# Optimization experiments

Hardware: AMD Instinct MI355X
Metric: run time of the kernel (lower is better)

Reference implementation:

```python
import jax, jax.numpy as jnp
import numpy as np

# block index -> upsample target resolution / whether self-attention is applied
RES = [32, 64, 256, 128, 64, 32, 16, 16, 32, 64, 128, 256]
ATTN = [False, False, False, False, False, True, True, True, True, False, False, False]
EPS = 1e-5


def conv5(x, w, b):
    # valid 5x5 conv, NCHW
    y = jax.lax.conv_general_dilated(x, w, (1, 1), 'VALID',
                                     dimension_numbers=('NCHW', 'OIHW', 'NCHW'))
    return y + b[None, :, None, None]


def up_nearest(x, size):
    # torch nn.Upsample(size) nearest: src_idx = floor(dst_idx * in / out)
    H, W = x.shape[2], x.shape[3]
    ri = (jnp.arange(size) * H) // size
    ci = (jnp.arange(size) * W) // size
    return x[:, :, ri][:, :, :, ci]


def norm_hw(x):
    # InstanceNorm2d(affine=False) == LayerNorm((H,W)) with identity affine:
    # normalize over spatial dims per (N, C), biased variance.
    m = x.mean((2, 3), keepdims=True)
    v = x.var((2, 3), keepdims=True)
    return (x - m) * jax.lax.rsqrt(v + EPS)


def norm_batch(x):
    # BatchNorm2d in training mode: batch statistics over (N, H, W) per channel.
    m = x.mean((0, 2, 3), keepdims=True)
    v = x.var((0, 2, 3), keepdims=True)
    return (x - m) * jax.lax.rsqrt(v + EPS)


def attention(x, qw, qb, kw, kb, vw, vb):
    B, C, H, W = x.shape
    q = (jnp.einsum('oc,bchw->bohw', qw, x) + qb[None, :, None, None]).reshape(B, C, H * W)
    k = (jnp.einsum('oc,bchw->bohw', kw, x) + kb[None, :, None, None]).reshape(B, C, H * W)
    v = (jnp.einsum('oc,bchw->bohw', vw, x) + vb[None, :, None, None]).reshape(B, C, H * W)
    # scores[b, m, n] = sum_c k[b, c, m] * q[b, c, n]; softmax over n
    a = jax.nn.softmax(jnp.einsum('bcm,bcn->bmn', k, q), axis=-1)  # [B, HW, HW]
    out = jnp.einsum('bcm,bmn->bcn', v, a).reshape(B, C, H, W)
    return out + x


def setup_inputs() -> dict:
    key = jax.random.key(0)
    k = jax.random.split(key, 22)
    s = 0.1
    f = jnp.float32
    return {
        'x': jax.random.normal(k[0], (32, 3, 256, 256), f),
        'noise_z': jax.random.normal(k[1], (1, 512), f),
        'lin_w': jax.random.normal(k[2], (768, 512), f) * 0.02,
        'lin_b': jax.random.normal(k[3], (768,), f) * 0.02,
        'conv_w': jax.random.normal(k[4], (12, 3, 3, 5, 5), f) * s,
        'conv_b': jax.random.normal(k[5], (12, 3), f) * s,
        'conv2_w': jax.random.normal(k[6], (12, 3, 3, 5, 5), f) * s,
        'conv2_b': jax.random.normal(k[7], (12, 3), f) * s,
        'q_w': jax.random.normal(k[8], (12, 3, 3), f) * s,
        'q_b': jax.random.normal(k[9], (12, 3), f) * s,
        'k_w': jax.random.normal(k[10], (12, 3, 3), f) * s,
        'k_b': jax.random.normal(k[11], (12, 3), f) * s,
        'v_w': jax.random.normal(k[12], (12, 3, 3), f) * s,
        'v_b': jax.random.normal(k[13], (12, 3), f) * s,
        'in_p': jax.random.uniform(k[14], (12, 3), f),
        'ln_p': jax.random.uniform(k[15], (12, 3), f),
        'bn_p': jax.random.uniform(k[16], (12, 3), f),
        'bn_w': jax.random.uniform(k[17], (12, 3), f),
        'bn_b': jax.random.uniform(k[18], (12, 3), f) * 0.1,
        'p1': jax.random.uniform(k[19], (12,), f),
        'p2': jax.random.uniform(k[20], (12,), f),
    }


def reference(x, noise_z, lin_w, lin_b, conv_w, conv_b, conv2_w, conv2_b,
              q_w, q_b, k_w, k_b, v_w, v_b, in_p, ln_p, bn_p, bn_w, bn_b, p1, p2):

    def block(i, h):
        r = RES[i]
        real = h
        y = up_nearest(conv5(real, conv_w[i], conv_b[i]), r)
        # InstanceNorm / LayerNorm (no affine) coincide here; BatchNorm has affine.
        inorm = norm_hw(y)
        bnorm = norm_batch(y) * bn_w[i][None, :, None, None] + bn_b[i][None, :, None, None]
        y2 = y + (jnp.sum(in_p[i]) + jnp.sum(ln_p[i])) * inorm + jnp.sum(bn_p[i]) * bnorm
        y2 = y2 * p1[i] + p2[i] * up_nearest(conv5(real, conv2_w[i], conv2_b[i]), r)
        if ATTN[i]:
            y2 = attention(y2, q_w[i], q_b[i], k_w[i], k_b[i], v_w[i], v_b[i])
        return y2

    # noise path: Linear(512 -> 768) -> (1, 3, 16, 16) -> ReesBlock(32) -> ReesBlock(64)
    n = (noise_z @ lin_w.T + lin_b).reshape(1, 3, 16, 16)
    n = block(0, n)
    n = block(1, n)  # (1, 3, 64, 64)

    a = x
    for i in range(2, 12):
        a = block(i, a)
        if i == 4:  # encoder index 2, resolution 64 -> add noise (broadcast over batch)
            a = a + n
    return jnp.tanh(a)
```

## Files before the change

kernel.cpp:

```cpp
#include <hip/hip_runtime.h>
#include <math.h>

#define EPS 1e-5f
#define LOG2E 1.44269504088896340736f

#define AS_GLOBAL __attribute__((address_space(1)))
#define AS_LDS    __attribute__((address_space(3)))

__device__ __forceinline__ float2 ab_from(float s1, float s2, float bs, float bs2,
    float hw, float Nf, float si_, float sb, float bnw_c, float bnb_c, float p1v) {
  float inv = 1.0f / hw;
  float mi = s1 * inv, vi = s2 * inv - mi * mi;
  float ri = rsqrtf(vi + EPS);
  float invb = 1.0f / (Nf * hw);
  float mb = bs * invb, vb = bs2 * invb - mb * mb;
  float rb = rsqrtf(vb + EPS);
  float A = 1.0f + si_ * ri + sb * rb * bnw_c;
  float B = -(si_ * ri * mi + sb * rb * bnw_c * mb) + sb * bnb_c;
  return make_float2(A * p1v, B * p1v);
}

__device__ __forceinline__ void compute_AB_P(
    const float* __restrict__ P, int n, int NT, int T, float hw, float Nf,
    const float* __restrict__ inp, const float* __restrict__ lnp,
    const float* __restrict__ bnp, const float* __restrict__ bnw,
    const float* __restrict__ bnb, const float* __restrict__ p1p,
    const float* __restrict__ p2p, float* pA, float* pB, float* pP2,
    float* sred ) {
  int t = threadIdx.x;
  if (t == 0) *pP2 = p2p[0];
  if (t < 192) {
    int c2 = t >> 5, l = t & 31;
    const float* pp = P + c2 * NT;
    float aAll = 0.f, aOwn = 0.f;
    int base = n * T;
    #pragma unroll 4
    for (int i = l; i < NT; i += 32) {
      float v = pp[i];
      aAll += v;
      if ((unsigned)(i - base) < (unsigned)T) aOwn += v;
    }
    #pragma unroll
    for (int off = 16; off; off >>= 1) {
      aAll += __shfl_down(aAll, off, 32);
      aOwn += __shfl_down(aOwn, off, 32);
    }
    if (l == 0) { sred[c2] = aOwn; sred[6 + c2] = aAll; }
  }
  __syncthreads();
  if (t < 3) {
    int c = t;
    float si_ = inp[0] + inp[1] + inp[2] + lnp[0] + lnp[1] + lnp[2];
    float sb = bnp[0] + bnp[1] + bnp[2];
    float2 ab = ab_from(sred[2 * c], sred[2 * c + 1], sred[6 + 2 * c],
                        sred[6 + 2 * c + 1], hw, Nf, si_, sb, bnw[c], bnb[c],
                        p1p[0]);
    pA[c] = ab.x;
    pB[c] = ab.y;
  }
  __syncthreads();
}

#define STATS_REDUCE_STORE(scv, sqv, sumsp, bidv)                             \
  {                                                                           \
    _Pragma("unroll")                                                         \
    for (int off = 32; off; off >>= 1) {                                      \
      _Pragma("unroll")                                                       \
      for (int c = 0; c < 3; ++c) {                                           \
        scv[c] += __shfl_down(scv[c], off);                                   \
        sqv[c] += __shfl_down(sqv[c], off);                                   \
      }                                                                       \
    }                                                                         \
    __shared__ float redS[4][3], redQ[4][3];                                  \
    int wid = threadIdx.x >> 6, lane = threadIdx.x & 63;                      \
    if (lane == 0) {                                                          \
      _Pragma("unroll")                                                       \
      for (int c = 0; c < 3; ++c) { redS[wid][c] = scv[c]; redQ[wid][c] = sqv[c]; } \
    }                                                                         \
    __syncthreads();                                                          \
    if (threadIdx.x < 3) {                                                    \
      int c = threadIdx.x;                                                    \
      int NTg = (int)gridDim.x;                                               \
      sumsp[(2 * c) * NTg + (bidv)] =                                         \
          redS[0][c] + redS[1][c] + redS[2][c] + redS[3][c];                  \
      sumsp[(2 * c + 1) * NTg + (bidv)] =                                     \
          redQ[0][c] + redQ[1][c] + redQ[2][c] + redQ[3][c];                  \
    }                                                                         \
  }

__device__ __forceinline__ int xcd_swz() {
// ... 54 lines not shown
    int gx2 = sx0 + col2; gx2 = gx2 < Hin ? gx2 : Hin - 1;
    int gy = sy0 + rr; gy = gy < Hin ? gy : Hin - 1;
    lin[(cc * IHv + rr) * IW + col2] =
        stage_val<MODE, IDENT>(inb, ps, pyu, pbase, Hin, gy, gx2, Sp, logrp,
                               pA, pB, pP2v, pnoise, cc);
  }
}

template <int SMODE, int THv>
__global__ __launch_bounds__(256) void conv_up_t(
    const float* __restrict__ in, const float2* __restrict__ pyu,
    float2* __restrict__ yu,
    const float* __restrict__ w1, const float* __restrict__ b1,
    const float* __restrict__ w2, const float* __restrict__ b2,
    float* __restrict__ sums, int Hin, int S, int r, int tilesX, int tilesY,
    const float* __restrict__ psums,
    const float* __restrict__ pinp, const float* __restrict__ plnp,
    const float* __restrict__ pbnp, const float* __restrict__ pbnw,
    const float* __restrict__ pbnb, const float* __restrict__ pp1,
    const float* __restrict__ pp2, const float* __restrict__ pnoise,
    int pN, int Sp, int logrp, int pNT, int pT) {
  const int TW = 64, IW = 68, IH = THv + 4, NH = THv / 16;
  __shared__ float lin[3 * IH * IW];
  __shared__ float pA[3], pB[3], pP2v, sred[12];
  int bid = xcd_swz();
  int tpi = tilesX * tilesY;
  int n = bid / tpi;
  int trem = bid - n * tpi;
  int tyB = trem / tilesX, txB = trem - tyB * tilesX;
  int px0 = txB * TW, py0 = tyB * THv;
  const float* inb = in + (size_t)n * 3 * Hin * Hin;
  if (SMODE == 1) {
    compute_AB_P(psums, n, pNT, pT, (float)(Hin * Hin), (float)pN, pinp, plnp,
                 pbnp, pbnw, pbnb, pp1, pp2, pA, pB, &pP2v, sred);
    size_t pbase = (size_t)n * 3 * Sp * Sp;
    stage_tile<1, false, IH>(lin, nullptr, 0, pyu, pbase, Hin, py0, px0, Sp,
                             logrp, pA, pB, pP2v, pnoise);
  } else if (SMODE == 3) {
    const float* smallb = in + (size_t)n * 3 * Sp * Sp;
    stage_tile<3, false, IH>(lin, smallb, 0, nullptr, 0, Hin, py0, px0, Sp,
                             logrp, nullptr, nullptr, 0.f, nullptr);
  } else {
    if (px0 + IW <= Hin && py0 + IH <= Hin) {
      for (int t4 = threadIdx.x; t4 < 3 * IH * 17; t4 += 256) {
        int cc = t4 / (IH * 17);
        int rem = t4 - cc * (IH * 17);
        int rr = rem / 17, j = rem - rr * 17;
        const float* src = inb + ((size_t)cc * Hin + py0 + rr) * Hin + px0 + 4 * j;
        int base = t4 - (threadIdx.x & 63);
// ... 71 lines not shown
        float2* yp = yu + idx;
        *reinterpret_cast<float4*>(yp) =
            make_float4(a1[h][c][0], a2[h][c][0], a1[h][c][1], a2[h][c][1]);
        *reinterpret_cast<float4*>(yp + 2) =
            make_float4(a1[h][c][2], a2[h][c][2], a1[h][c][3], a2[h][c][3]);
        #pragma unroll
        for (int x = 0; x < 4; ++x) {
          float wgt = wy * wx[x];
          sc[c] += a1[h][c][x] * wgt;
          sq[c] += a1[h][c][x] * a1[h][c][x] * wgt;
        }
      }
    }
  }
  STATS_REDUCE_STORE(sc, sq, sums, bid)
}

template <int SMODE, bool IDENT, int THv>
__global__ __launch_bounds__(256) void conv_dn_t(
    const float* __restrict__ in, const float2* __restrict__ pyu,
    float2* __restrict__ yu,
    const float* __restrict__ w1, const float* __restrict__ b1,
    const float* __restrict__ w2, const float* __restrict__ b2,
    float* __restrict__ sums, int Hin, int S, int hc, int logr,
    int tilesX, int tilesY,
    const float* __restrict__ psums,
    const float* __restrict__ pinp, const float* __restrict__ plnp,
    const float* __restrict__ pbnp, const float* __restrict__ pbnw,
    const float* __restrict__ pbnb, const float* __restrict__ pp1,
    const float* __restrict__ pp2, const float* __restrict__ pnoise,
    int pN, int Sp, int logrp, int pNT, int pT) {
  const int TW = 32, IW = 68, IH = (THv == 16) ? 36 : 20, NH = THv / 8;
  __shared__ float lin[3 * IH * IW];
  __shared__ float pA[3], pB[3], pP2v, sred[12];
  int bid = xcd_swz();
  int tpi = tilesX * tilesY;
  int n = bid / tpi;
  int trem = bid - n * tpi;
  int tyB = trem / tilesX, txB = trem - tyB * tilesX;
  int px0 = txB * TW, py0 = tyB * THv;
  int sy0 = (py0 * hc) >> logr, sx0 = (px0 * hc) >> logr;
  const float* inb = in + (size_t)n * 3 * Hin * Hin;
  if (SMODE == 1) {
    compute_AB_P(psums, n, pNT, pT, (float)(Hin * Hin), (float)pN, pinp, plnp,
                 pbnp, pbnw, pbnb, pp1, pp2, pA, pB, &pP2v, sred);
    size_t pbase = (size_t)n * 3 * Sp * Sp;
    stage_tile<1, IDENT, IH>(lin, nullptr, 0, pyu, pbase, Hin, sy0, sx0, Sp,
                             logrp, pA, pB, pP2v, pnoise);
  } else if (SMODE == 2) {
    size_t ps = (size_t)96 * Hin * Hin;
    stage_tile<2, false, IH>(lin, inb, ps, nullptr, 0, Hin, sy0, sx0, 0, 0,
                             nullptr, nullptr, 0.f, nullptr);
  } else {
    stage_tile<0, false, IH>(lin, inb, 0, nullptr, 0, Hin, sy0, sx0, 0, 0,
                             nullptr, nullptr, 0.f, nullptr);
  }
  __syncthreads();
  int tx = threadIdx.x & 31, ty = threadIdx.x >> 5;
  int px = px0 + tx;
  int sxl = ((px * hc) >> logr) - sx0;
  int pys[NH], syl[NH];
  #pragma unroll
  for (int h = 0; h < NH; ++h) {
    pys[h] = py0 + ty + 8 * h;
    syl[h] = ((pys[h] * hc) >> logr) - sy0;
  }
  float a1[NH][3], a2[NH][3];
  #pragma unroll
  for (int h = 0; h < NH; ++h)
    #pragma unroll
    for (int c = 0; c < 3; ++c) { a1[h][c] = b1[c]; a2[h][c] = b2[c]; }
  #pragma unroll
  for (int ci = 0; ci < 3; ++ci) {
    const float* wp1 = w1 + ci * 25;
    const float* wp2 = w2 + ci * 25;
    #pragma unroll
    for (int h = 0; h < NH; ++h) {
      const float* lrow = lin + (ci * IH + syl[h]) * IW + sxl;
      #pragma unroll
      for (int ky = 0; ky < 5; ++ky) {
        float v[5];
        #pragma unroll
        for (int j = 0; j < 5; ++j) v[j] = lrow[ky * IW + j];
        #pragma unroll
        for (int c = 0; c < 3; ++c) {
          #pragma unroll
          for (int kx = 0; kx < 5; ++kx) {
            a1[h][c] = fmaf(v[kx], wp1[c * 75 + ky * 5 + kx], a1[h][c]);
            a2[h][c] = fmaf(v[kx], wp2[c * 75 + ky * 5 + kx], a2[h][c]);
          }
        }
      }
    }
  }
  float sc[3] = {0.f, 0.f, 0.f}, sq[3] = {0.f, 0.f, 0.f};
  #pragma unroll
  for (int h = 0; h < NH; ++h) {
    bool valid = (pys[h] < S) && (px < S);
    if (valid) {
      #pragma unroll
      for (int c = 0; c < 3; ++c) {
        size_t idx = ((size_t)(n * 3 + c) * S + pys[h]) * S + px;
        yu[idx] = make_float2(a1[h][c], a2[h][c]);
        sc[c] += a1[h][c];
        sq[c] += a1[h][c] * a1[h][c];
      }
    }
  }
  STATS_REDUCE_STORE(sc, sq, sums, bid)
}

__global__ __launch_bounds__(256) void linear_wave(
    const float* __restrict__ z, const float* __restrict__ w,
    const float* __restrict__ b, float* __restrict__ out) {
  int row = (blockIdx.x << 2) + (threadIdx.x >> 6);
  int lane = threadIdx.x & 63;
  const float4* wr = reinterpret_cast<const float4*>(w + (size_t)row * 512);
  const float4* zz = reinterpret_cast<const float4*>(z);
  float acc = 0.f;
  #pragma unroll
  for (int i = 0; i < 2; ++i) {
    float4 wv = wr[lane + 64 * i];
    float4 zv = zz[lane + 64 * i];
    acc += wv.x * zv.x + wv.y * zv.y + wv.z * zv.z + wv.w * zv.w;
// ... 139 lines not shown
    }
    __syncthreads();
  }
  {
    float P2b = p2p[1];
    for (int t = tid; t < 12288; t += 256) {
      int c = t >> 12, p = t & 4095;
      int oy = p >> 6, ox = p & 63;
      int si = ((oy * 28) >> 6) * 28 + ((ox * 28) >> 6);
      nb0[t] = AB[c] * ys1[c * 784 + si] + AB[3 + c] + P2b * u21[c * 784 + si];
    }
  }
}

__global__ __launch_bounds__(256) void attn_rows_f(
    const float2* __restrict__ yu, const float* __restrict__ sums,
    const float* __restrict__ inp, const float* __restrict__ lnp,
    const float* __restrict__ bnp, const float* __restrict__ bnw,
    const float* __restrict__ bnb, const float* __restrict__ p1p,
    const float* __restrict__ p2p,
    const float* __restrict__ qw, const float* __restrict__ qb,
    const float* __restrict__ kw, const float* __restrict__ kb,
    float* __restrict__ Mp, float* __restrict__ Lp, int S,
    int pNT, int pT) {
  __shared__ float pA[3], pB[3], pP2v, sred[12];
  __shared__ __align__(16) float y2s[768], qs[768];
  int bid = blockIdx.x;
  int np = bid & 3; bid >>= 2;
  int mc = bid & 3;
  int b = bid >> 2;
  compute_AB_P(sums, b, pNT, pT, 1024.f, 32.f, inp, lnp, bnp, bnw, bnb, p1p,
               p2p, pA, pB, &pP2v, sred);
  size_t ybase = (size_t)b * 3 * S * S;
  for (int t = threadIdx.x; t < 768; t += 256) {
    int c = t >> 8, j = t & 255;
    int n = (np << 8) + j;
    int oy = n >> 5, ox = n & 31;
    int si = ((oy * S) >> 5) * S + ((ox * S) >> 5);
    float2 v = yu[ybase + c * S * S + si];
    y2s[t] = pA[c] * v.x + pB[c] + pP2v * v.y;
  }
  __syncthreads();
  for (int t = threadIdx.x; t < 768; t += 256) {
    int o = t >> 8, j = t & 255;
    qs[t] = qb[o] + qw[o * 3] * y2s[j] + qw[o * 3 + 1] * y2s[256 + j] +
            qw[o * 3 + 2] * y2s[512 + j];
  }
// ... 27 lines not shown
  #pragma unroll 4
  for (int j = 0; j < 64; ++j) {
    float4 qa = qa4[j], qbv = qb4[j], qc = qc4[j];
    float s0 = k0 * qa.x + k1 * qbv.x + k2 * qc.x;
    float s1 = k0 * qa.y + k1 * qbv.y + k2 * qc.y;
    float s2 = k0 * qa.z + k1 * qbv.z + k2 * qc.z;
    float s3 = k0 * qa.w + k1 * qbv.w + k2 * qc.w;
    l += exp2f(s0 - mr) + exp2f(s1 - mr) + exp2f(s2 - mr) + exp2f(s3 - mr);
  }
  int idx = (b * 4 + np) * 1024 + m;
  Mp[idx] = mr;
  Lp[idx] = l;
}

__global__ __launch_bounds__(256) void attn_out_f(
    const float2* __restrict__ yu, const float* __restrict__ sums,
    const float* __restrict__ inp, const float* __restrict__ lnp,
    const float* __restrict__ bnp, const float* __restrict__ bnw,
    const float* __restrict__ bnb, const float* __restrict__ p1p,
    const float* __restrict__ p2p,
    const float* __restrict__ qw, const float* __restrict__ qb,
    const float* __restrict__ kw, const float* __restrict__ kb,
    const float* __restrict__ vw, const float* __restrict__ vb,
    const float* __restrict__ Mp, const float* __restrict__ Lp,
    float* __restrict__ aout, int S, int pNT, int pT) {
  __shared__ float pA[3], pB[3], pP2v, sred[12];
  __shared__ __align__(16) float ym[768], ks[768], vs[768], Ms[256], Ls[256];
  int bid = blockIdx.x;
  int mp = bid & 3; bid >>= 2;
  int nc = bid & 3;
  int b = bid >> 2;
  compute_AB_P(sums, b, pNT, pT, 1024.f, 32.f, inp, lnp, bnp, bnw, bnb, p1p,
               p2p, pA, pB, &pP2v, sred);
  size_t ybase = (size_t)b * 3 * S * S;
  for (int t = threadIdx.x; t < 768; t += 256) {
    int c = t >> 8, j = t & 255;
    int m = (mp << 8) + j;
    int oy = m >> 5, ox = m & 31;
    int si = ((oy * S) >> 5) * S + ((ox * S) >> 5);
    float2 v = yu[ybase + c * S * S + si];
    ym[t] = pA[c] * v.x + pB[c] + pP2v * v.y;
  }
  __syncthreads();
  for (int t = threadIdx.x; t < 768; t += 256) {
    int o = t >> 8, j = t & 255;
    float y0 = ym[j], y1 = ym[256 + j], y2v = ym[512 + j];
    ks[t] = (kb[o] + kw[o * 3] * y0 + kw[o * 3 + 1] * y1 + kw[o * 3 + 2] * y2v) * LOG2E;
    vs[t] = vb[o] + vw[o * 3] * y0 + vw[o * 3 + 1] * y1 + vw[o * 3 + 2] * y2v;
// ... 48 lines not shown
    s = ka.z * q0 + kbv.z * q1 + kc.z * q2;
    w = exp2f(s - mm.z) * ll.z;
    a0 = fmaf(va.z, w, a0); a1 = fmaf(vbv.z, w, a1); a2 = fmaf(vc.z, w, a2);
    s = ka.w * q0 + kbv.w * q1 + kc.w * q2;
    w = exp2f(s - mm.w) * ll.w;
    a0 = fmaf(va.w, w, a0); a1 = fmaf(vbv.w, w, a1); a2 = fmaf(vc.w, w, a2);
  }
  if (mp == 0) { a0 += yn[0]; a1 += yn[1]; a2 += yn[2]; }
  size_t o0 = (size_t)mp * 98304 + (size_t)b * 3072 + n;
  aout[o0] = a0;
  aout[o0 + 1024] = a1;
  aout[o0 + 2048] = a2;
}

__global__ __launch_bounds__(1024) void attn256_conv(
    const float2* __restrict__ yu, const float* __restrict__ sums,
    const float* __restrict__ inp, const float* __restrict__ lnp,
    const float* __restrict__ bnp, const float* __restrict__ bnw,
    const float* __restrict__ bnb, const float* __restrict__ p1p,
    const float* __restrict__ p2p,
    const float* __restrict__ qw, const float* __restrict__ qb,
    const float* __restrict__ kw, const float* __restrict__ kb,
    const float* __restrict__ vw, const float* __restrict__ vb,
    const float* __restrict__ cw1, const float* __restrict__ cb1,
    const float* __restrict__ cw2, const float* __restrict__ cb2,
    float2* __restrict__ yu_out, float* __restrict__ sums_out, int S, int r,
    int pNT, int pT) {
  __shared__ float pA[3], pB[3], pP2v, sred[12];
  __shared__ __align__(16) float y2s[768], qs[768], ks[768], vs[768];
  __shared__ __align__(16) float Ms[256], Ls[256];
  __shared__ float Mq[1024], Lq[1024];
  __shared__ float Oq[3072];
  __shared__ float redS[16][3], redQ[16][3];
  int tid = threadIdx.x;
  int quarter = tid >> 8;
  int lane256 = tid & 255;
  int b = blockIdx.x;
  compute_AB_P(sums, b, pNT, pT, 256.f, 32.f, inp, lnp, bnp, bnw, bnb, p1p,
               p2p, pA, pB, &pP2v, sred);
  size_t ybase = (size_t)b * 3 * S * S;
  if (tid < 768) {
    int c = tid >> 8, p = tid & 255;
    int oy = p >> 4, ox = p & 15;
    int si = ((oy * S) >> 4) * S + ((ox * S) >> 4);
    float2 v = yu[ybase + c * S * S + si];
    y2s[tid] = pA[c] * v.x + pB[c] + pP2v * v.y;
  }
  __syncthreads();
  if (tid < 768) {
    int o = tid >> 8, p = tid & 255;
    float y0 = y2s[p], y1 = y2s[256 + p], y2v = y2s[512 + p];
    qs[tid] = qb[o] + qw[o * 3] * y0 + qw[o * 3 + 1] * y1 + qw[o * 3 + 2] * y2v;
    ks[tid] = (kb[o] + kw[o * 3] * y0 + kw[o * 3 + 1] * y1 + kw[o * 3 + 2] * y2v) * LOG2E;
    vs[tid] = vb[o] + vw[o * 3] * y0 + vw[o * 3 + 1] * y1 + vw[o * 3 + 2] * y2v;
// ... 126 lines not shown
  int wid = tid >> 6, lane = tid & 63;
  if (lane == 0) {
    #pragma unroll
    for (int c = 0; c < 3; ++c) { redS[wid][c] = sc[c]; redQ[wid][c] = sq[c]; }
  }
  __syncthreads();
  if (tid < 3) {
    int c = tid;
    float s1 = 0.f, s2 = 0.f;
    #pragma unroll
    for (int w = 0; w < 16; ++w) { s1 += redS[w][c]; s2 += redQ[w][c]; }
    int NTg = (int)gridDim.x;
    sums_out[(2 * c) * NTg + b] = s1;
    sums_out[(2 * c + 1) * NTg + b] = s2;
  }
}

__global__ __launch_bounds__(256) void attn144(
    const float2* __restrict__ yu, const float* __restrict__ sums,
    const float* __restrict__ inp, const float* __restrict__ lnp,
    const float* __restrict__ bnp, const float* __restrict__ bnw,
    const float* __restrict__ bnb, const float* __restrict__ p1p,
    const float* __restrict__ p2p,
    const float* __restrict__ qw, const float* __restrict__ qb,
    const float* __restrict__ kw, const float* __restrict__ kb,
    const float* __restrict__ vw, const float* __restrict__ vb,
    float* __restrict__ O) {
  __shared__ float pA[3], pB[3], pP2v, sred[12];
  __shared__ float y2[432], qs[432], ks[432], vs[432];
  __shared__ float Ms[144], Ls[144], wn[144];
  int b = blockIdx.x;
  int tid = threadIdx.x;
  compute_AB_P(sums, b, 32, 1, 1024.f, 32.f, inp, lnp, bnp, bnw, bnb, p1p,
               p2p, pA, pB, &pP2v, sred);
  for (int t = tid; t < 432; t += 256) {
    int c = t / 144, j = t - c * 144;
    float2 v = yu[((size_t)b * 3 + c) * 144 + j];
    y2[t] = pA[c] * v.x + pB[c] + pP2v * v.y;
  }
  __syncthreads();
  if (tid < 144) {
    int j = tid;
    float y0 = y2[j], y1 = y2[144 + j], y2v = y2[288 + j];
    #pragma unroll
    for (int o = 0; o < 3; ++o) {
      qs[o * 144 + j] = qb[o] + qw[o * 3] * y0 + qw[o * 3 + 1] * y1 + qw[o * 3 + 2] * y2v;
      ks[o * 144 + j] = (kb[o] + kw[o * 3] * y0 + kw[o * 3 + 1] * y1 + kw[o * 3 + 2] * y2v) * LOG2E;
      vs[o * 144 + j] = vb[o] + vw[o * 3] * y0 + vw[o * 3 + 1] * y1 + vw[o * 3 + 2] * y2v;
    }
// ... 27 lines not shown
    for (int m = 0; m < 144; ++m) {
      float s = ks[m] * q0 + ks[144 + m] * q1 + ks[288 + m] * q2;
      float w = wn[m] * exp2f(s - Ms[m]) * Ls[m];
      a0 = fmaf(vs[m], w, a0);
      a1 = fmaf(vs[144 + m], w, a1);
      a2 = fmaf(vs[288 + m], w, a2);
    }
    size_t ob = (size_t)b * 432;
    O[ob + nq] = a0 + y2[nq];
    O[ob + 144 + nq] = a1 + y2[144 + nq];
    O[ob + 288 + nq] = a2 + y2[288 + nq];
  }
}

__global__ __launch_bounds__(256) void elem_final(
    const float2* __restrict__ yu, const float* __restrict__ sums,
    const float* __restrict__ inp, const float* __restrict__ lnp,
    const float* __restrict__ bnp, const float* __restrict__ bnw,
    const float* __restrict__ bnb, const float* __restrict__ p1p,
    const float* __restrict__ p2p, float* __restrict__ out, int S,
    int pNT, int pT) {
  __shared__ float pA[3], pB[3], pP2v, sred[12];
  int bid = xcd_swz();
  int n = bid >> 8;
  int p = ((bid & 255) << 8) + threadIdx.x;
  compute_AB_P(sums, n, pNT, pT, 65536.f, 32.f, inp, lnp, bnp, bnw, bnb, p1p,
               p2p, pA, pB, &pP2v, sred);
  int oy = p >> 8, ox = p & 255;
  int si = ((oy * S) >> 8) * S + ((ox * S) >> 8);
  size_t ybase = (size_t)n * 3 * S * S;
  #pragma unroll
  for (int c = 0; c < 3; ++c) {
    float2 v = yu[ybase + c * S * S + si];
    out[((size_t)(n * 3 + c) << 16) + p] = tanhf(pA[c] * v.x + pB[c] + pP2v * v.y);
  }
}

#define NPX nullptr, nullptr, nullptr, nullptr, nullptr, nullptr, nullptr, \
            nullptr, nullptr, 0, 0, 0, 0, 0

extern "C" void kernel_launch(void* const* d_in, const int* in_sizes, int n_in,
                              void* d_out, int out_size, void* d_ws, size_t ws_size,
                              hipStream_t stream) {
  const float* x       = (const float*)d_in[0];
  const float* noise_z = (const float*)d_in[1];
  const float* lin_w   = (const float*)d_in[2];
  const float* lin_b   = (const float*)d_in[3];
  const float* conv_w  = (const float*)d_in[4];
  const float* conv_b  = (const float*)d_in[5];
  const float* conv2_w = (const float*)d_in[6];
  const float* conv2_b = (const float*)d_in[7];
  const float* q_w     = (const float*)d_in[8];
  const float* q_b     = (const float*)d_in[9];
  const float* k_w     = (const float*)d_in[10];
  const float* k_b     = (const float*)d_in[11];
  const float* v_w     = (const float*)d_in[12];
  const float* v_b     = (const float*)d_in[13];
  const float* in_p    = (const float*)d_in[14];
  const float* ln_p    = (const float*)d_in[15];
  const float* bn_p    = (const float*)d_in[16];
  const float* bn_w    = (const float*)d_in[17];
  const float* bn_b    = (const float*)d_in[18];
  const float* p1      = (const float*)d_in[19];
  const float* p2      = (const float*)d_in[20];
  float* out = (float*)d_out;

  float* ws = (float*)d_ws;
  size_t off = 0;
  auto alloc = [&](size_t nf) { float* p = ws + off; off += nf; return p; };
  float* PS   = alloc(21120);
  float* PS2  = PS;
  float* PS3  = PS + 6144;
  float* PS4  = PS + 12288;
  float* PS5  = PS + 15360;
  float* PS6  = PS + 16128;
  float* PS6a = PS + 16512;
  float* PS7a = PS + 16704;
  float* PS9  = PS + 16896;
  float* PS10 = PS + 17280;
  float* PS11 = PS + 18048;
  float* P45  = alloc(393216);
  float* O144 = alloc(13824);
  float2* YU2 = (float2*)alloc(12192768);
  float2* PA  = (float2*)alloc(3145728);
  float2* PB  = (float2*)alloc(3145728);
  float* Mp   = alloc(131072);
  float* Lp   = alloc(131072);
  float* NB0  = alloc(12288);
  float* LIN  = alloc(768);

  const float* nul = nullptr;
  const float2* nul2 = nullptr;

  linear_wave<<<192, 256, 0, stream>>>(noise_z, lin_w, lin_b, LIN);
  noise_rest<<<1, 256, 0, stream>>>(LIN, conv_w, conv_b, conv2_w, conv2_b,
      in_p, ln_p, bn_p, bn_w, bn_b, p1, p2, NB0);

  conv_up_t<0, 32><<<1024, 256, 0, stream>>>(x, nul2, YU2, conv_w + 450,
      conv_b + 6, conv2_w + 450, conv2_b + 6, PS2, 256, 252, 256, 4, 8,
      NPX);
  conv_dn_t<1, false, 16><<<1024, 256, 0, stream>>>(nul, YU2, PA,
      conv_w + 675, conv_b + 9, conv2_w + 675, conv2_b + 9, PS3,
      256, 128, 252, 7, 4, 8,
      PS2, in_p + 6, ln_p + 6, bn_p + 6, bn_w + 6, bn_b + 6, p1 + 2,
      p2 + 2, nul, 32, 252, 8, 1024, 32);
  conv_dn_t<1, true, 8><<<512, 256, 0, stream>>>(nul, PA, PB,
      conv_w + 900, conv_b + 12, conv2_w + 900, conv2_b + 12, PS4,
      128, 64, 124, 6, 2, 8,
      PS3, in_p + 9, ln_p + 9, bn_p + 9, bn_w + 9, bn_b + 9, p1 + 3,
      p2 + 3, nul, 32, 128, 7, 1024, 32);
  conv_dn_t<1, true, 8><<<128, 256, 0, stream>>>(nul, PB, PA,
      conv_w + 1125, conv_b + 15, conv2_w + 1125, conv2_b + 15, PS5,
      64, 32, 60, 5, 1, 4,
      PS4, in_p + 12, ln_p + 12, bn_p + 12, bn_w + 12, bn_b + 12, p1 + 4,
      p2 + 4, NB0, 32, 64, 6, 512, 16);
  attn_rows_f<<<512, 256, 0, stream>>>(PA, PS5, in_p + 15, ln_p + 15,
      bn_p + 15, bn_w + 15, bn_b + 15, p1 + 5, p2 + 5,
      q_w + 45, q_b + 15, k_w + 45, k_b + 15, Mp, Lp, 32, 128, 4);
  attn_out_f<<<512, 256, 0, stream>>>(PA, PS5, in_p + 15, ln_p + 15,
      bn_p + 15, bn_w + 15, bn_b + 15, p1 + 5, p2 + 5,
      q_w + 45, q_b + 15, k_w + 45, k_b + 15, v_w + 45, v_b + 15, Mp, Lp, P45,
      32, 128, 4);
  conv_dn_t<2, false, 8><<<64, 256, 0, stream>>>(P45, nul2, PB,
      conv_w + 1350, conv_b + 18, conv2_w + 1350, conv2_b + 18, PS6,
      32, 16, 28, 4, 1, 2, NPX);
  attn256_conv<<<32, 1024, 0, stream>>>(PB, PS6, in_p + 18, ln_p + 18,
      bn_p + 18, bn_w + 18, bn_b + 18, p1 + 6, p2 + 6,
      q_w + 54, q_b + 18, k_w + 54, k_b + 18, v_w + 54, v_b + 18,
      conv_w + 1575, conv_b + 21, conv2_w + 1575, conv2_b + 21,
      PA, PS6a, 16, 16, 64, 2);
  attn256_conv<<<32, 1024, 0, stream>>>(PA, PS6a, in_p + 21, ln_p + 21,
      bn_p + 21, bn_w + 21, bn_b + 21, p1 + 7, p2 + 7,
      q_w + 63, q_b + 21, k_w + 63, k_b + 21, v_w + 63, v_b + 21,
      conv_w + 1800, conv_b + 24, conv2_w + 1800, conv2_b + 24,
      PB, PS7a, 12, 32, 32, 1);
  attn144<<<32, 256, 0, stream>>>(PB, PS7a, in_p + 24, ln_p + 24,
      bn_p + 24, bn_w + 24, bn_b + 24, p1 + 8, p2 + 8,
      q_w + 72, q_b + 24, k_w + 72, k_b + 24, v_w + 72, v_b + 24, O144);
  conv_up_t<3, 16><<<64, 256, 0, stream>>>(O144, nul2, PA, conv_w + 2025,
      conv_b + 27, conv2_w + 2025, conv2_b + 27, PS9, 32, 28, 64, 1, 2,
      nullptr, nullptr, nullptr, nullptr, nullptr, nullptr, nullptr,
      nullptr, nullptr, 0, 12, 5, 0, 0);
  conv_up_t<1, 16><<<128, 256, 0, stream>>>(nul, PA, PB, conv_w + 2250,
      conv_b + 30, conv2_w + 2250, conv2_b + 30, PS10, 64, 60, 128, 1, 4,
      PS9, in_p + 27, ln_p + 27, bn_p + 27, bn_w + 27, bn_b + 27,
      p1 + 9, p2 + 9, nul, 32, 28, 6, 64, 2);
  conv_up_t<1, 16><<<512, 256, 0, stream>>>(nul, PB, YU2, conv_w + 2475,
      conv_b + 33, conv2_w + 2475, conv2_b + 33, PS11, 128, 124, 256, 2, 8,
      PS10, in_p + 30, ln_p + 30, bn_p + 30, bn_w + 30, bn_b + 30,
      p1 + 10, p2 + 10, nul, 32, 60, 7, 128, 4);
  elem_final<<<8192, 256, 0, stream>>>(YU2, PS11, in_p + 33, ln_p + 33,
      bn_p + 33, bn_w + 33, bn_b + 33, p1 + 11, p2 + 11, out, 124, 512, 16);
}
```

Baseline: 434.1 us.

## Finalize norm coefficients in last block via atomic ticket instead of per-block reduction

Each producer kernel now uses an atomic ticket so that its last finishing block reduces the per-tile statistics and writes per-sample A/B coefficients to a small buffer. Consumer kernels just load six floats instead of having every block re-reduce the full partial-sum array. The 256-res downsample conv also drops its 16-row tile variant in favor of 8-row tiles over twice as many blocks. This adds a threadfence, an atomic and a memset, and puts a serial tail on one block per kernel.

```diff
diff --git a/kernel.cpp b/kernel.cpp
--- a/kernel.cpp
+++ b/kernel.cpp
@@ -20,46 +20,56 @@
   return make_float2(A * p1v, B * p1v);
 }
 
-__device__ __forceinline__ void compute_AB_P(
-    const float* __restrict__ P, int n, int NT, int T, float hw, float Nf,
-    const float* __restrict__ inp, const float* __restrict__ lnp,
-    const float* __restrict__ bnp, const float* __restrict__ bnw,
-    const float* __restrict__ bnb, const float* __restrict__ p1p,
-    const float* __restrict__ p2p, float* pA, float* pB, float* pP2,
-    float* sred ) {
+__device__ __forceinline__ void load_AB(const float* __restrict__ ABt, int n,
+    const float* __restrict__ p2p, float* pA, float* pB, float* pP2) {
   int t = threadIdx.x;
-  if (t == 0) *pP2 = p2p[0];
+  if (t < 3) pA[t] = ABt[n * 6 + t];
+  else if (t < 6) pB[t - 3] = ABt[n * 6 + t];
+  else if (t == 6) *pP2 = p2p[0];
+  __syncthreads();
+}
+
+__device__ __forceinline__ void finalize_AB(
+    const float* __restrict__ PS_, int NT, int T, float hw,
+    const float* __restrict__ finp, const float* __restrict__ flnp,
+    const float* __restrict__ fbnp, const float* __restrict__ fbnw,
+    const float* __restrict__ fbnb, const float* __restrict__ fp1,
+    float* __restrict__ ABout, float* sn ) {
+  int t = threadIdx.x;
   if (t < 192) {
-    int c2 = t >> 5, l = t & 31;
-    const float* pp = P + c2 * NT;
-    float aAll = 0.f, aOwn = 0.f;
-    int base = n * T;
-    #pragma unroll 4
-    for (int i = l; i < NT; i += 32) {
-      float v = pp[i];
-      aAll += v;
-      if ((unsigned)(i - base) < (unsigned)T) aOwn += v;
-    }
-    #pragma unroll
-    for (int off = 16; off; off >>= 1) {
-      aAll += __shfl_down(aAll, off, 32);
-      aOwn += __shfl_down(aOwn, off, 32);
-    }
-    if (l == 0) { sred[c2] = aOwn; sred[6 + c2] = aAll; }
-  }
-  __syncthreads();
-  if (t < 3) {
-    int c = t;
-    float si_ = inp[0] + inp[1] + inp[2] + lnp[0] + lnp[1] + lnp[2];
-    float sb = bnp[0] + bnp[1] + bnp[2];
-    float2 ab = ab_from(sred[2 * c], sred[2 * c + 1], sred[6 + 2 * c],
-                        sred[6 + 2 * c + 1], hw, Nf, si_, sb, bnw[c], bnb[c],
-                        p1p[0]);
-    pA[c] = ab.x;
-    pB[c] = ab.y;
-  }
-  __syncthreads();
-}
+    int c2 = t >> 5, n = t & 31;
+    const float* pp = PS_ + c2 * NT + n * T;
+    float s = 0.f;
+    #pragma unroll 2
+    for (int i = 0; i < T; ++i) s += pp[i];
+    sn[c2 * 32 + n] = s;
+    float bsum = s;
+    #pragma unroll
+    for (int off = 16; off; off >>= 1) bsum += __shfl_down(bsum, off, 32);
+    if (n == 0) sn[192 + c2] = bsum;
+  }
+  __syncthreads();
+  if (t < 128) {
+    int n = t >> 2, c = t & 3;
+    if (c < 3) {
+      float si_ = finp[0] + finp[1] + finp[2] + flnp[0] + flnp[1] + flnp[2];
+      float sb = fbnp[0] + fbnp[1] + fbnp[2];
+      float2 ab = ab_from(sn[2 * c * 32 + n], sn[(2 * c + 1) * 32 + n],
+                          sn[192 + 2 * c], sn[192 + 2 * c + 1],
+                          hw, 32.f, si_, sb, fbnw[c], fbnb[c], fp1[0]);
+      ABout[n * 6 + c] = ab.x;
+      ABout[n * 6 + 3 + c] = ab.y;
+    }
+  }
+}
+
+#define TICKET_LAST(ticket, lastf)                                            \
+  __syncthreads();                                                            \
+  if (threadIdx.x == 0) {                                                     \
+    __threadfence();                                                          \
+    lastf = (atomicAdd((ticket), 1) == (int)gridDim.x - 1);                   \
+  }                                                                           \
+  __syncthreads();
 
 #define STATS_REDUCE_STORE(scv, sqv, sumsp, bidv)                             \
   {                                                                           \
@@ -73,7 +83,7 @@
     }                                                                         \
     __shared__ float redS[4][3], redQ[4][3];                                  \
     int wid = threadIdx.x >> 6, lane = threadIdx.x & 63;                      \
-    if (lane == 0) {                                                          \
+    if (lane == 0 && wid < 4) {                                               \
       _Pragma("unroll")                                                       \
       for (int c = 0; c < 3; ++c) { redS[wid][c] = scv[c]; redQ[wid][c] = sqv[c]; } \
     }                                                                         \
@@ -158,15 +168,16 @@
     const float* __restrict__ w1, const float* __restrict__ b1,
     const float* __restrict__ w2, const float* __restrict__ b2,
     float* __restrict__ sums, int Hin, int S, int r, int tilesX, int tilesY,
-    const float* __restrict__ psums,
-    const float* __restrict__ pinp, const float* __restrict__ plnp,
-    const float* __restrict__ pbnp, const float* __restrict__ pbnw,
-    const float* __restrict__ pbnb, const float* __restrict__ pp1,
-    const float* __restrict__ pp2, const float* __restrict__ pnoise,
-    int pN, int Sp, int logrp, int pNT, int pT) {
+    const float* __restrict__ ABin, const float* __restrict__ pp2,
+    const float* __restrict__ pnoise, int Sp, int logrp,
+    const float* __restrict__ finp, const float* __restrict__ flnp,
+    const float* __restrict__ fbnp, const float* __restrict__ fbnw,
+    const float* __restrict__ fbnb, const float* __restrict__ fp1,
+    float* __restrict__ ABout, int* __restrict__ ticket) {
   const int TW = 64, IW = 68, IH = THv + 4, NH = THv / 16;
   __shared__ float lin[3 * IH * IW];
-  __shared__ float pA[3], pB[3], pP2v, sred[12];
+  __shared__ float pA[3], pB[3], pP2v;
+  __shared__ int lastf;
   int bid = xcd_swz();
   int tpi = tilesX * tilesY;
   int n = bid / tpi;
@@ -175,8 +186,7 @@
   int px0 = txB * TW, py0 = tyB * THv;
   const float* inb = in + (size_t)n * 3 * Hin * Hin;
   if (SMODE == 1) {
-    compute_AB_P(psums, n, pNT, pT, (float)(Hin * Hin), (float)pN, pinp, plnp,
-                 pbnp, pbnw, pbnb, pp1, pp2, pA, pB, &pP2v, sred);
+    load_AB(ABin, n, pp2, pA, pB, &pP2v);
     size_t pbase = (size_t)n * 3 * Sp * Sp;
     stage_tile<1, false, IH>(lin, nullptr, 0, pyu, pbase, Hin, py0, px0, Sp,
                              logrp, pA, pB, pP2v, pnoise);
@@ -278,9 +288,15 @@
     }
   }
   STATS_REDUCE_STORE(sc, sq, sums, bid)
-}
-
-template <int SMODE, bool IDENT, int THv>
+  TICKET_LAST(ticket, lastf)
+  if (lastf) {
+    __threadfence();
+    finalize_AB(sums, (int)gridDim.x, (int)gridDim.x >> 5, (float)(r * r),
+                finp, flnp, fbnp, fbnw, fbnb, fp1, ABout, lin);
+  }
+}
+
+template <int SMODE, bool IDENT>
 __global__ __launch_bounds__(256) void conv_dn_t(
     const float* __restrict__ in, const float2* __restrict__ pyu,
     float2* __restrict__ yu,
@@ -288,26 +304,26 @@
     const float* __restrict__ w2, const float* __restrict__ b2,
     float* __restrict__ sums, int Hin, int S, int hc, int logr,
     int tilesX, int tilesY,
-    const float* __restrict__ psums,
-    const float* __restrict__ pinp, const float* __restrict__ plnp,
-    const float* __restrict__ pbnp, const float* __restrict__ pbnw,
-    const float* __restrict__ pbnb, const float* __restrict__ pp1,
-    const float* __restrict__ pp2, const float* __restrict__ pnoise,
-    int pN, int Sp, int logrp, int pNT, int pT) {
-  const int TW = 32, IW = 68, IH = (THv == 16) ? 36 : 20, NH = THv / 8;
+    const float* __restrict__ ABin, const float* __restrict__ pp2,
+    const float* __restrict__ pnoise, int Sp, int logrp,
+    const float* __restrict__ finp, const float* __restrict__ flnp,
+    const float* __restrict__ fbnp, const float* __restrict__ fbnw,
+    const float* __restrict__ fbnb, const float* __restrict__ fp1,
+    float* __restrict__ ABout, int* __restrict__ ticket) {
+  const int TW = 32, TH = 8, IW = 68, IH = 20;
   __shared__ float lin[3 * IH * IW];
-  __shared__ float pA[3], pB[3], pP2v, sred[12];
+  __shared__ float pA[3], pB[3], pP2v;
+  __shared__ int lastf;
   int bid = xcd_swz();
   int tpi = tilesX * tilesY;
   int n = bid / tpi;
   int trem = bid - n * tpi;
   int tyB = trem / tilesX, txB = trem - tyB * tilesX;
-  int px0 = txB * TW, py0 = tyB * THv;
+  int px0 = txB * TW, py0 = tyB * TH;
   int sy0 = (py0 * hc) >> logr, sx0 = (px0 * hc) >> logr;
   const float* inb = in + (size_t)n * 3 * Hin * Hin;
   if (SMODE == 1) {
-    compute_AB_P(psums, n, pNT, pT, (float)(Hin * Hin), (float)pN, pinp, plnp,
-                 pbnp, pbnw, pbnb, pp1, pp2, pA, pB, &pP2v, sred);
+    load_AB(ABin, n, pp2, pA, pB, &pP2v);
     size_t pbase = (size_t)n * 3 * Sp * Sp;
     stage_tile<1, IDENT, IH>(lin, nullptr, 0, pyu, pbase, Hin, sy0, sx0, Sp,
                              logrp, pA, pB, pP2v, pnoise);
@@ -321,57 +337,50 @@
   }
   __syncthreads();
   int tx = threadIdx.x & 31, ty = threadIdx.x >> 5;
-  int px = px0 + tx;
+  int px = px0 + tx, py = py0 + ty;
   int sxl = ((px * hc) >> logr) - sx0;
-  int pys[NH], syl[NH];
+  int syl = ((py * hc) >> logr) - sy0;
+  float a1[3], a2[3];
   #pragma unroll
-  for (int h = 0; h < NH; ++h) {
-    pys[h] = py0 + ty + 8 * h;
-    syl[h] = ((pys[h] * hc) >> logr) - sy0;
-  }
-  float a1[NH][3], a2[NH][3];
-  #pragma unroll
-  for (int h = 0; h < NH; ++h)
-    #pragma unroll
-    for (int c = 0; c < 3; ++c) { a1[h][c] = b1[c]; a2[h][c] = b2[c]; }
+  for (int c = 0; c < 3; ++c) { a1[c] = b1[c]; a2[c] = b2[c]; }
   #pragma unroll
   for (int ci = 0; ci < 3; ++ci) {
+    const float* lrow = lin + (ci * IH + syl) * IW + sxl;
     const float* wp1 = w1 + ci * 25;
     const float* wp2 = w2 + ci * 25;
     #pragma unroll
-    for (int h = 0; h < NH; ++h) {
-      const float* lrow = lin + (ci * IH + syl[h]) * IW + sxl;
-      #pragma unroll
-      for (int ky = 0; ky < 5; ++ky) {
-        float v[5];
+    for (int ky = 0; ky < 5; ++ky) {
+      float v[5];
+      #pragma unroll
+      for (int j = 0; j < 5; ++j) v[j] = lrow[ky * IW + j];
+      #pragma unroll
+      for (int c = 0; c < 3; ++c) {
         #pragma unroll
-        for (int j = 0; j < 5; ++j) v[j] = lrow[ky * IW + j];
-        #pragma unroll
-        for (int c = 0; c < 3; ++c) {
-          #pragma unroll
-          for (int kx = 0; kx < 5; ++kx) {
-            a1[h][c] = fmaf(v[kx], wp1[c * 75 + ky * 5 + kx], a1[h][c]);
-            a2[h][c] = fmaf(v[kx], wp2[c * 75 + ky * 5 + kx], a2[h][c]);
-          }
+        for (int kx = 0; kx < 5; ++kx) {
+          a1[c] = fmaf(v[kx], wp1[c * 75 + ky * 5 + kx], a1[c]);
+          a2[c] = fmaf(v[kx], wp2[c * 75 + ky * 5 + kx], a2[c]);
         }
       }
     }
   }
   float sc[3] = {0.f, 0.f, 0.f}, sq[3] = {0.f, 0.f, 0.f};
-  #pragma unroll
-  for (int h = 0; h < NH; ++h) {
-    bool valid = (pys[h] < S) && (px < S);
-    if (valid) {
-      #pragma unroll
-      for (int c = 0; c < 3; ++c) {
-        size_t idx = ((size_t)(n * 3 + c) * S + pys[h]) * S + px;
-        yu[idx] = make_float2(a1[h][c], a2[h][c]);
-        sc[c] += a1[h][c];
-        sq[c] += a1[h][c] * a1[h][c];
-      }
+  bool valid = (py < S) && (px < S);
+  if (valid) {
+    #pragma unroll
+    for (int c = 0; c < 3; ++c) {
+      size_t idx = ((size_t)(n * 3 + c) * S + py) * S + px;
+      yu[idx] = make_float2(a1[c], a2[c]);
+      sc[c] += a1[c];
+      sq[c] += a1[c] * a1[c];
     }
   }
   STATS_REDUCE_STORE(sc, sq, sums, bid)
+  TICKET_LAST(ticket, lastf)
+  if (lastf) {
+    __threadfence();
+    finalize_AB(sums, (int)gridDim.x, (int)gridDim.x >> 5, (float)(S * S),
+                finp, flnp, fbnp, fbnw, fbnb, fp1, ABout, lin);
+  }
 }
 
 __global__ __launch_bounds__(256) void linear_wave(
@@ -541,23 +550,18 @@
 }
 
 __global__ __launch_bounds__(256) void attn_rows_f(
-    const float2* __restrict__ yu, const float* __restrict__ sums,
-    const float* __restrict__ inp, const float* __restrict__ lnp,
-    const float* __restrict__ bnp, const float* __restrict__ bnw,
-    const float* __restrict__ bnb, const float* __restrict__ p1p,
-    const float* __restrict__ p2p,
+    const float2* __restrict__ yu, const float* __restrict__ ABin,
+    const float* __restrict__ pp2,
     const float* __restrict__ qw, const float* __restrict__ qb,
     const float* __restrict__ kw, const float* __restrict__ kb,
-    float* __restrict__ Mp, float* __restrict__ Lp, int S,
-    int pNT, int pT) {
-  __shared__ float pA[3], pB[3], pP2v, sred[12];
+    float* __restrict__ Mp, float* __restrict__ Lp, int S) {
+  __shared__ float pA[3], pB[3], pP2v;
   __shared__ __align__(16) float y2s[768], qs[768];
   int bid = blockIdx.x;
   int np = bid & 3; bid >>= 2;
   int mc = bid & 3;
   int b = bid >> 2;
-  compute_AB_P(sums, b, pNT, pT, 1024.f, 32.f, inp, lnp, bnp, bnw, bnb, p1p,
-               p2p, pA, pB, &pP2v, sred);
+  load_AB(ABin, b, pp2, pA, pB, &pP2v);
   size_t ybase = (size_t)b * 3 * S * S;
   for (int t = threadIdx.x; t < 768; t += 256) {
     int c = t >> 8, j = t & 255;
@@ -615,24 +619,20 @@
 }
 
 __global__ __launch_bounds__(256) void attn_out_f(
-    const float2* __restrict__ yu, const float* __restrict__ sums,
-    const float* __restrict__ inp, const float* __restrict__ lnp,
-    const float* __restrict__ bnp, const float* __restrict__ bnw,
-    const float* __restrict__ bnb, const float* __restrict__ p1p,
-    const float* __restrict__ p2p,
+    const float2* __restrict__ yu, const float* __restrict__ ABin,
+    const float* __restrict__ pp2,
     const float* __restrict__ qw, const float* __restrict__ qb,
     const float* __restrict__ kw, const float* __restrict__ kb,
     const float* __restrict__ vw, const float* __restrict__ vb,
     const float* __restrict__ Mp, const float* __restrict__ Lp,
-    float* __restrict__ aout, int S, int pNT, int pT) {
-  __shared__ float pA[3], pB[3], pP2v, sred[12];
+    float* __restrict__ aout, int S) {
+  __shared__ float pA[3], pB[3], pP2v;
   __shared__ __align__(16) float ym[768], ks[768], vs[768], Ms[256], Ls[256];
   int bid = blockIdx.x;
   int mp = bid & 3; bid >>= 2;
   int nc = bid & 3;
   int b = bid >> 2;
-  compute_AB_P(sums, b, pNT, pT, 1024.f, 32.f, inp, lnp, bnp, bnw, bnb, p1p,
-               p2p, pA, pB, &pP2v, sred);
+  load_AB(ABin, b, pp2, pA, pB, &pP2v);
   size_t ybase = (size_t)b * 3 * S * S;
   for (int t = threadIdx.x; t < 768; t += 256) {
     int c = t >> 8, j = t & 255;
@@ -711,30 +711,30 @@
 }
 
 __global__ __launch_bounds__(1024) void attn256_conv(
-    const float2* __restrict__ yu, const float* __restrict__ sums,
-    const float* __restrict__ inp, const float* __restrict__ lnp,
-    const float* __restrict__ bnp, const float* __restrict__ bnw,
-    const float* __restrict__ bnb, const float* __restrict__ p1p,
-    const float* __restrict__ p2p,
+    const float2* __restrict__ yu, const float* __restrict__ ABin,
+    const float* __restrict__ pp2,
     const float* __restrict__ qw, const float* __restrict__ qb,
     const float* __restrict__ kw, const float* __restrict__ kb,
     const float* __restrict__ vw, const float* __restrict__ vb,
     const float* __restrict__ cw1, const float* __restrict__ cb1,
     const float* __restrict__ cw2, const float* __restrict__ cb2,
     float2* __restrict__ yu_out, float* __restrict__ sums_out, int S, int r,
-    int pNT, int pT) {
-  __shared__ float pA[3], pB[3], pP2v, sred[12];
+    const float* __restrict__ finp, const float* __restrict__ flnp,
+    const float* __restrict__ fbnp, const float* __restrict__ fbnw,
+    const float* __restrict__ fbnb, const float* __restrict__ fp1,
+    float* __restrict__ ABout, int* __restrict__ ticket) {
+  __shared__ float pA[3], pB[3], pP2v;
   __shared__ __align__(16) float y2s[768], qs[768], ks[768], vs[768];
   __shared__ __align__(16) float Ms[256], Ls[256];
   __shared__ float Mq[1024], Lq[1024];
   __shared__ float Oq[3072];
   __shared__ float redS[16][3], redQ[16][3];
+  __shared__ int lastf;
   int tid = threadIdx.x;
   int quarter = tid >> 8;
   int lane256 = tid & 255;
   int b = blockIdx.x;
-  compute_AB_P(sums, b, pNT, pT, 256.f, 32.f, inp, lnp, bnp, bnw, bnb, p1p,
-               p2p, pA, pB, &pP2v, sred);
+  load_AB(ABin, b, pp2, pA, pB, &pP2v);
   size_t ybase = (size_t)b * 3 * S * S;
   if (tid < 768) {
     int c = tid >> 8, p = tid & 255;
@@ -891,25 +891,27 @@
     sums_out[(2 * c) * NTg + b] = s1;
     sums_out[(2 * c + 1) * NTg + b] = s2;
   }
+  TICKET_LAST(ticket, lastf)
+  if (lastf) {
+    __threadfence();
+    finalize_AB(sums_out, (int)gridDim.x, 1, (float)(r * r),
+                finp, flnp, fbnp, fbnw, fbnb, fp1, ABout, Oq);
+  }
 }
 
 __global__ __launch_bounds__(256) void attn144(
-    const float2* __restrict__ yu, const float* __restrict__ sums,
-    const float* __restrict__ inp, const float* __restrict__ lnp,
-    const float* __restrict__ bnp, const float* __restrict__ bnw,
-    const float* __restrict__ bnb, const float* __restrict__ p1p,
-    const float* __restrict__ p2p,
+    const float2* __restrict__ yu, const float* __restrict__ ABin,
+    const float* __restrict__ pp2,
     const float* __restrict__ qw, const float* __restrict__ qb,
     const float* __restrict__ kw, const float* __restrict__ kb,
     const float* __restrict__ vw, const float* __restrict__ vb,
     float* __restrict__ O) {
-  __shared__ float pA[3], pB[3], pP2v, sred[12];
+  __shared__ float pA[3], pB[3], pP2v;
   __shared__ float y2[432], qs[432], ks[432], vs[432];
   __shared__ float Ms[144], Ls[144], wn[144];
   int b = blockIdx.x;
   int tid = threadIdx.x;
-  compute_AB_P(sums, b, 32, 1, 1024.f, 32.f, inp, lnp, bnp, bnw, bnb, p1p,
-               p2p, pA, pB, &pP2v, sred);
+  load_AB(ABin, b, pp2, pA, pB, &pP2v);
   for (int t = tid; t < 432; t += 256) {
     int c = t / 144, j = t - c * 144;
     float2 v = yu[((size_t)b * 3 + c) * 144 + j];
@@ -967,18 +969,13 @@
 }
 
 __global__ __launch_bounds__(256) void elem_final(
-    const float2* __restrict__ yu, const float* __restrict__ sums,
-    const float* __restrict__ inp, const float* __restrict__ lnp,
-    const float* __restrict__ bnp, const float* __restrict__ bnw,
-    const float* __restrict__ bnb, const float* __restrict__ p1p,
-    const float* __restrict__ p2p, float* __restrict__ out, int S,
-    int pNT, int pT) {
-  __shared__ float pA[3], pB[3], pP2v, sred[12];
+    const float2* __restrict__ yu, const float* __restrict__ ABin,
+    const float* __restrict__ pp2, float* __restrict__ out, int S) {
+  __shared__ float pA[3], pB[3], pP2v;
   int bid = xcd_swz();
   int n = bid >> 8;
   int p = ((bid & 255) << 8) + threadIdx.x;
-  compute_AB_P(sums, n, pNT, pT, 65536.f, 32.f, inp, lnp, bnp, bnw, bnb, p1p,
-               p2p, pA, pB, &pP2v, sred);
+  load_AB(ABin, n, pp2, pA, pB, &pP2v);
   int oy = p >> 8, ox = p & 255;
   int si = ((oy * S) >> 8) * S + ((ox * S) >> 8);
   size_t ybase = (size_t)n * 3 * S * S;
@@ -988,9 +985,6 @@
     out[((size_t)(n * 3 + c) << 16) + p] = tanhf(pA[c] * v.x + pB[c] + pP2v * v.y);
   }
 }
-
-#define NPX nullptr, nullptr, nullptr, nullptr, nullptr, nullptr, nullptr, \
-            nullptr, nullptr, 0, 0, 0, 0, 0
 
 extern "C" void kernel_launch(void* const* d_in, const int* in_sizes, int n_in,
                               void* d_out, int out_size, void* d_ws, size_t ws_size,
@@ -1021,17 +1015,29 @@
   float* ws = (float*)d_ws;
   size_t off = 0;
   auto alloc = [&](size_t nf) { float* p = ws + off; off += nf; return p; };
-  float* PS   = alloc(21120);
-  float* PS2  = PS;
-  float* PS3  = PS + 6144;
-  float* PS4  = PS + 12288;
-  float* PS5  = PS + 15360;
-  float* PS6  = PS + 16128;
-  float* PS6a = PS + 16512;
-  float* PS7a = PS + 16704;
-  float* PS9  = PS + 16896;
-  float* PS10 = PS + 17280;
-  float* PS11 = PS + 18048;
+  float* PS    = alloc(27264);
+  float* PS2   = PS;
+  float* PS3   = PS + 6144;
+  float* PS4   = PS + 18432;
+  float* PS5   = PS + 21504;
+  float* PS6   = PS + 22272;
+  float* PS6a  = PS + 22656;
+  float* PS7a  = PS + 22848;
+  float* PS9   = PS + 23040;
+  float* PS10  = PS + 23424;
+  float* PS11  = PS + 24192;
+  float* AB    = alloc(1920);
+  float* AB2   = AB;
+  float* AB3   = AB + 192;
+  float* AB4   = AB + 384;
+  float* AB5   = AB + 576;
+  float* AB6   = AB + 768;
+  float* AB6a  = AB + 960;
+  float* AB7a  = AB + 1152;
+  float* AB9   = AB + 1344;
+  float* AB10  = AB + 1536;
+  float* AB11  = AB + 1728;
+  int*   TICK  = (int*)alloc(16);
   float* P45  = alloc(393216);
   float* O144 = alloc(13824);
   float2* YU2 = (float2*)alloc(12192768);
@@ -1042,6 +1048,8 @@
   float* NB0  = alloc(12288);
   float* LIN  = alloc(768);
 
+  hipMemsetAsync(TICK, 0, 16 * sizeof(int), stream);
+
   const float* nul = nullptr;
   const float2* nul2 = nullptr;
 
@@ -1051,57 +1059,55 @@
 
   conv_up_t<0, 32><<<1024, 256, 0, stream>>>(x, nul2, YU2, conv_w + 450,
       conv_b + 6, conv2_w + 450, conv2_b + 6, PS2, 256, 252, 256, 4, 8,
-      NPX);
-  conv_dn_t<1, false, 16><<<1024, 256, 0, stream>>>(nul, YU2, PA,
+      nul, nul, nul, 0, 0,
+      in_p + 6, ln_p + 6, bn_p + 6, bn_w + 6, bn_b + 6, p1 + 2, AB2, TICK + 0);
+  conv_dn_t<1, false><<<2048, 256, 0, stream>>>(nul, YU2, PA,
       conv_w + 675, conv_b + 9, conv2_w + 675, conv2_b + 9, PS3,
-      256, 128, 252, 7, 4, 8,
-      PS2, in_p + 6, ln_p + 6, bn_p + 6, bn_w + 6, bn_b + 6, p1 + 2,
-      p2 + 2, nul, 32, 252, 8, 1024, 32);
-  conv_dn_t<1, true, 8><<<512, 256, 0, stream>>>(nul, PA, PB,
+      256, 128, 252, 7, 4, 16,
+      AB2, p2 + 2, nul, 252, 8,
+      in_p + 9, ln_p + 9, bn_p + 9, bn_w + 9, bn_b + 9, p1 + 3, AB3, TICK + 1);
+  conv_dn_t<1, true><<<512, 256, 0, stream>>>(nul, PA, PB,
       conv_w + 900, conv_b + 12, conv2_w + 900, conv2_b + 12, PS4,
       128, 64, 124, 6, 2, 8,
-      PS3, in_p + 9, ln_p + 9, bn_p + 9, bn_w + 9, bn_b + 9, p1 + 3,
-      p2 + 3, nul, 32, 128, 7, 1024, 32);
-  conv_dn_t<1, true, 8><<<128, 256, 0, stream>>>(nul, PB, PA,
+      AB3, p2 + 3, nul, 128, 7,
+      in_p + 12, ln_p + 12, bn_p + 12, bn_w + 12, bn_b + 12, p1 + 4, AB4, TICK + 2);
+  conv_dn_t<1, true><<<128, 256, 0, stream>>>(nul, PB, PA,
       conv_w + 1125, conv_b + 15, conv2_w + 1125, conv2_b + 15, PS5,
       64, 32, 60, 5, 1, 4,
-      PS4, in_p + 12, ln_p + 12, bn_p + 12, bn_w + 12, bn_b + 12, p1 + 4,
-      p2 + 4, NB0, 32, 64, 6, 512, 16);
-  attn_rows_f<<<512, 256, 0, stream>>>(PA, PS5, in_p + 15, ln_p + 15,
-      bn_p + 15, bn_w + 15, bn_b + 15, p1 + 5, p2 + 5,
-      q_w + 45, q_b + 15, k_w + 45, k_b + 15, Mp, Lp, 32, 128, 4);
-  attn_out_f<<<512, 256, 0, stream>>>(PA, PS5, in_p + 15, ln_p + 15,
-      bn_p + 15, bn_w + 15, bn_b + 15, p1 + 5, p2 + 5,
-      q_w + 45, q_b + 15, k_w + 45, k_b + 15, v_w + 45, v_b + 15, Mp, Lp, P45,
-      32, 128, 4);
-  conv_dn_t<2, false, 8><<<64, 256, 0, stream>>>(P45, nul2, PB,
+      AB4, p2 + 4, NB0, 64, 6,
+      in_p + 15, ln_p + 15, bn_p + 15, bn_w + 15, bn_b + 15, p1 + 5, AB5, TICK + 3);
+  attn_rows_f<<<512, 256, 0, stream>>>(PA, AB5, p2 + 5,
+      q_w + 45, q_b + 15, k_w + 45, k_b + 15, Mp, Lp, 32);
+  attn_out_f<<<512, 256, 0, stream>>>(PA, AB5, p2 + 5,
+      q_w + 45, q_b + 15, k_w + 45, k_b + 15, v_w + 45, v_b + 15, Mp, Lp, P45, 32);
+  conv_dn_t<2, false><<<64, 256, 0, stream>>>(P45, nul2, PB,
       conv_w + 1350, conv_b + 18, conv2_w + 1350, conv2_b + 18, PS6,
-      32, 16, 28, 4, 1, 2, NPX);
-  attn256_conv<<<32, 1024, 0, stream>>>(PB, PS6, in_p + 18, ln_p + 18,
-      bn_p + 18, bn_w + 18, bn_b + 18, p1 + 6, p2 + 6,
+      32, 16, 28, 4, 1, 2,
+      nul, nul, nul, 0, 0,
+      in_p + 18, ln_p + 18, bn_p + 18, bn_w + 18, bn_b + 18, p1 + 6, AB6, TICK + 4);
+  attn256_conv<<<32, 1024, 0, stream>>>(PB, AB6, p2 + 6,
       q_w + 54, q_b + 18, k_w + 54, k_b + 18, v_w + 54, v_b + 18,
       conv_w + 1575, conv_b + 21, conv2_w + 1575, conv2_b + 21,
-      PA, PS6a, 16, 16, 64, 2);
-  attn256_conv<<<32, 1024, 0, stream>>>(PA, PS6a, in_p + 21, ln_p + 21,
-      bn_p + 21, bn_w + 21, bn_b + 21, p1 + 7, p2 + 7,
+      PA, PS6a, 16, 16,
+      in_p + 21, ln_p + 21, bn_p + 21, bn_w + 21, bn_b + 21, p1 + 7, AB6a, TICK + 5);
+  attn256_conv<<<32, 1024, 0, stream>>>(PA, AB6a, p2 + 7,
       q_w + 63, q_b + 21, k_w + 63, k_b + 21, v_w + 63, v_b + 21,
       conv_w + 1800, conv_b + 24, conv2_w + 1800, conv2_b + 24,
-      PB, PS7a, 12, 32, 32, 1);
-  attn144<<<32, 256, 0, stream>>>(PB, PS7a, in_p + 24, ln_p + 24,
-      bn_p + 24, bn_w + 24, bn_b + 24, p1 + 8, p2 + 8,
+      PB, PS7a, 12, 32,
+      in_p + 24, ln_p + 24, bn_p + 24, bn_w + 24, bn_b + 24, p1 + 8, AB7a, TICK + 6);
+  attn144<<<32, 256, 0, stream>>>(PB, AB7a, p2 + 8,
       q_w + 72, q_b + 24, k_w + 72, k_b + 24, v_w + 72, v_b + 24, O144);
   conv_up_t<3, 16><<<64, 256, 0, stream>>>(O144, nul2, PA, conv_w + 2025,
       conv_b + 27, conv2_w + 2025, conv2_b + 27, PS9, 32, 28, 64, 1, 2,
-      nullptr, nullptr, nullptr, nullptr, nullptr, nullptr, nullptr,
-      nullptr, nullptr, 0, 12, 5, 0, 0);
+      nul, nul, nul, 12, 5,
+      in_p + 27, ln_p + 27, bn_p + 27, bn_w + 27, bn_b + 27, p1 + 9, AB9, TICK + 7);
   conv_up_t<1, 16><<<128, 256, 0, stream>>>(nul, PA, PB, conv_w + 2250,
       conv_b + 30, conv2_w + 2250, conv2_b + 30, PS10, 64, 60, 128, 1, 4,
-      PS9, in_p + 27, ln_p + 27, bn_p + 27, bn_w + 27, bn_b + 27,
-      p1 + 9, p2 + 9, nul, 32, 28, 6, 64, 2);
+      AB9, p2 + 9, nul, 28, 6,
+      in_p + 30, ln_p + 30, bn_p + 30, bn_w + 30, bn_b + 30, p1 + 10, AB10, TICK + 8);
   conv_up_t<1, 16><<<512, 256, 0, stream>>>(nul, PB, YU2, conv_w + 2475,
       conv_b + 33, conv2_w + 2475, conv2_b + 33, PS11, 128, 124, 256, 2, 8,
-      PS10, in_p + 30, ln_p + 30, bn_p + 30, bn_w + 30, bn_b + 30,
-      p1 + 10, p2 + 10, nul, 32, 60, 7, 128, 4);
-  elem_final<<<8192, 256, 0, stream>>>(YU2, PS11, in_p + 33, ln_p + 33,
-      bn_p + 33, bn_w + 33, bn_b + 33, p1 + 11, p2 + 11, out, 124, 512, 16);
-}
+      AB10, p2 + 10, nul, 60, 7,
+      in_p + 33, ln_p + 33, bn_p + 33, bn_w + 33, bn_b + 33, p1 + 11, AB11, TICK + 9);
+  elem_final<<<8192, 256, 0, stream>>>(YU2, AB11, p2 + 11, out, 124);
+}
```

After: 653.9 us. 50.6% more time.
